# Optimization experiments

Measured on AMD Instinct MI355X. Metric: run time of the kernel, lower is better.

Reference implementation:

```python
import jax, jax.numpy as jnp
import numpy as np

KAPPA = 5.0
EPS_NORM = 1e-12  # torch F.normalize eps
EPS_LOG = 1e-09


def setup_inputs() -> dict:
    key = jax.random.key(0)
    student_output = jax.random.normal(key, (16384, 256), dtype=jnp.float32)
    return {"student_output": student_output}


def reference(student_output) -> jnp.ndarray:
    # L2-normalize rows (matches F.normalize: x / max(||x||, eps))
    norm = jnp.linalg.norm(student_output, axis=-1, keepdims=True)
    x_norm = student_output / jnp.maximum(norm, EPS_NORM)
    # pairwise cosine similarity [n, n]
    sim = x_norm @ x_norm.T
    kernel = jnp.exp(KAPPA * sim)
    density_estimates = kernel.sum(axis=1)  # [n]
    entropy = -jnp.mean(jnp.log(density_estimates + EPS_LOG))
    return entropy
```

## Files before the change

### kernel.cpp

```cpp
#include <hip/hip_runtime.h>


#define NROWS 16384
#define KDIM 256
#define NTILE 128
#define NT (NROWS / NTILE)
#define NSTRIP 8
#define TOTAL_BLOCKS (NT * NSTRIP)

#define SQRT_KLOG2E 2.68579577857f

typedef int i32x4_t __attribute__((ext_vector_type(4)));
typedef int i32x8_t __attribute__((ext_vector_type(8)));
typedef float f32x16_t __attribute__((ext_vector_type(16)));
typedef __attribute__((address_space(1))) const void global_cvoid_t;
typedef __attribute__((address_space(3))) void lds_void_t;

#if __has_builtin(__builtin_amdgcn_exp2f)
#define EXP2(x) __builtin_amdgcn_exp2f(x)
#else
#define EXP2(x) exp2f(x)
#endif

union frag8 { i32x8_t v8; i32x4_t v4[2]; };

__global__ __launch_bounds__(256)
void kde_normalize(const float* __restrict__ X, unsigned int* __restrict__ Xn8,
                   float* __restrict__ density, unsigned int* __restrict__ ticket) {
  const int wave = threadIdx.x >> 6;
  const int lane = threadIdx.x & 63;
  const int row = blockIdx.x * 4 + wave;
  const float4 v = ((const float4*)(X + (size_t)row * KDIM))[lane];
  float ss = v.x * v.x + v.y * v.y + v.z * v.z + v.w * v.w;
  ss += __shfl_xor(ss, 1);
  ss += __shfl_xor(ss, 2);
  ss += __shfl_xor(ss, 4);
  ss += __shfl_xor(ss, 8);
  ss += __shfl_xor(ss, 16);
  ss += __shfl_xor(ss, 32);
  const float scale = SQRT_KLOG2E / fmaxf(sqrtf(ss), 1e-12f);
  int p = 0;
  p = __builtin_amdgcn_cvt_pk_fp8_f32(v.x * scale, v.y * scale, p, false);
  p = __builtin_amdgcn_cvt_pk_fp8_f32(v.z * scale, v.w * scale, p, true);
  Xn8[(size_t)row * 64 + lane] = (unsigned int)p;
  if (threadIdx.x < 4) density[blockIdx.x * 4 + threadIdx.x] = 0.0f;
  if (blockIdx.x == 0 && threadIdx.x == 0) *ticket = 0u;
}

__global__ __launch_bounds__(512, 4)
void kde_gemm(const unsigned char* __restrict__ Xn8, float* __restrict__ density,
              unsigned int* __restrict__ ticket, float* __restrict__ out) {
  extern __shared__ char smem[];
  char* buf = smem;

  const int tid = threadIdx.x;
  const int wave = tid >> 6;
  const int lane = tid & 63;
  const int wr = wave >> 1;
  const int wc = wave & 1;
  const int m32 = lane & 31;
  const int h = lane >> 5;
  const int bi = blockIdx.x;
  const int s = blockIdx.y;
  const int t0 = s * 8;
  const int nt = (s == 0 && bi < NT / 2) ? 9 : 8;
  const char* Xb = (const char*)Xn8;

#define STAGE(base_row)                                                           \
  for (int c = wave; c < 32; c += 8) {                                            \
    const int rt = c >> 3, kb = (c >> 1) & 3, hh = c & 1;                         \
    const size_t gofs =                                                           \
        (size_t)((base_row) + rt * 32 + m32) * KDIM + kb * 64 + h * 32 + hh * 16; \
    __builtin_amdgcn_global_load_lds((global_cvoid_t*)(Xb + gofs),                \
                                     (lds_void_t*)(buf + c * 1024), 16, 0, 0);    \
  }

  STAGE(bi * NTILE);
  __syncthreads();
  frag8 areg[4];
#pragma unroll
  for (int kb = 0; kb < 4; kb++) {
    const char* pa = buf + (wr * 8 + kb * 2) * 1024 + lane * 16;
    areg[kb].v4[0] = *(const i32x4_t*)pa;
    areg[kb].v4[1] = *(const i32x4_t*)(pa + 1024);
  }
  __syncthreads();

  float rs[16];
#pragma unroll
  for (int r = 0; r < 16; r++) rs[r] = 0.0f;

  for (int k = 0; k < nt; ++k) {
    const int t = (k == 8) ? 64 : t0 + k;
    const int J = (bi + t) & (NT - 1);

    STAGE(J * NTILE);
    __syncthreads();

    f32x16_t acc[2];
#pragma unroll
    for (int j = 0; j < 2; j++) acc[j] = (f32x16_t)0.0f;

#pragma unroll
    for (int kb = 0; kb < 4; ++kb) {
      frag8 bf[2];
#pragma unroll
      for (int j = 0; j < 2; j++) {
        const char* pb = buf + ((wc * 2 + j) * 8 + kb * 2) * 1024 + lane * 16;
        bf[j].v4[0] = *(const i32x4_t*)pb;
        bf[j].v4[1] = *(const i32x4_t*)(pb + 1024);
      }
#pragma unroll
      for (int j = 0; j < 2; j++)
        acc[j] = __builtin_amdgcn_mfma_scale_f32_32x32x64_f8f6f4(
            areg[kb].v8, bf[j].v8, acc[j], 0, 0, 0, 127, 0, 127);
    }

    float c0 = 0.0f, c1 = 0.0f;
#pragma unroll
    for (int r = 0; r < 16; r++) {
      const float e0 = EXP2(acc[0][r]);
      const float e1 = EXP2(acc[1][r]);
      rs[r] += e0 + e1;
      c0 += e0;
      c1 += e1;
    }

    if (t != 0) {
      c0 += __shfl_xor(c0, 32);
      c1 += __shfl_xor(c1, 32);
      if (h == 0) {
        atomicAdd(&density[J * NTILE + wc * 64 + m32], c0);
        atomicAdd(&density[J * NTILE + wc * 64 + 32 + m32], c1);
      }
    }

    __syncthreads();
  }

#pragma unroll
  for (int r = 0; r < 16; r++) {
    float v = rs[r];
    v += __shfl_xor(v, 1);
    v += __shfl_xor(v, 2);
    v += __shfl_xor(v, 4);
    v += __shfl_xor(v, 8);
    v += __shfl_xor(v, 16);
    if (m32 == 0) {
      const int row = bi * NTILE + wr * 32 + (r & 3) + 8 * (r >> 2) + 4 * h;
      atomicAdd(&density[row], v);
    }
  }
#undef STAGE

  __syncthreads();
  if (tid == 0) {
    __threadfence();
    ((volatile unsigned int*)smem)[0] = atomicAdd(ticket, 1u);
  }
  __syncthreads();
  if (((volatile unsigned int*)smem)[0] == TOTAL_BLOCKS - 1) {
    __threadfence();
    float ssum = 0.0f;
    for (int i = tid; i < NROWS; i += 512) {
      const float d = __hip_atomic_load(&density[i], __ATOMIC_RELAXED,
                                        __HIP_MEMORY_SCOPE_AGENT);
      ssum += logf(d + 1e-9f);
    }
    ssum += __shfl_xor(ssum, 1);
    ssum += __shfl_xor(ssum, 2);
    ssum += __shfl_xor(ssum, 4);
    ssum += __shfl_xor(ssum, 8);
    ssum += __shfl_xor(ssum, 16);
    ssum += __shfl_xor(ssum, 32);
    float* red = ((float*)smem) + 16;
    if (lane == 0) red[wave] = ssum;
    __syncthreads();
    if (tid == 0) {
      float tot = 0.0f;
      for (int w = 0; w < 8; w++) tot += red[w];
      out[0] = -tot / (float)NROWS;
    }
  }
}

extern "C" void kernel_launch(void* const* d_in, const int* in_sizes, int n_in,
                              void* d_out, int out_size, void* d_ws, size_t ws_size,
                              hipStream_t stream) {
  const float* X = (const float*)d_in[0];
  float* out = (float*)d_out;
  char* ws = (char*)d_ws;
  unsigned int* Xn8 = (unsigned int*)ws;
  float* density = (float*)(ws + (size_t)NROWS * KDIM);
  unsigned int* ticket = (unsigned int*)(density + NROWS);

  hipFuncSetAttribute((const void*)kde_gemm,
                      hipFuncAttributeMaxDynamicSharedMemorySize, 32768);

  kde_normalize<<<NROWS / 4, 256, 0, stream>>>(X, Xn8, density, ticket);
  kde_gemm<<<dim3(NT, NSTRIP), 512, 32768, stream>>>((const unsigned char*)ws,
                                                     density, ticket, out);
}
```

Measured before the change: 142.5 us.

## Use 256-row A tiles per block with double-buffered B staging

Each block now holds a 256-row A tile, with two wave groups of 128 rows each, and streams 128-row B tiles through two LDS buffers. The next tile is prefetched while the current one is computed, so the per-iteration stage-then-sync stall goes away. This reuses every staged B tile across twice as many A rows and halves the grid to 64x8 blocks. The symmetric triangle schedule is recomputed with per-group activity and diagonal masks. In exchange, LDS use doubles to 64KB, which may lower occupancy, and the triangle bookkeeping grows more complex.

```diff
diff --git a/kernel.cpp b/kernel.cpp
--- a/kernel.cpp
+++ b/kernel.cpp
@@ -3,10 +3,9 @@
 
 #define NROWS 16384
 #define KDIM 256
-#define NTILE 128
-#define NT (NROWS / NTILE)
+#define NT 128
 #define NSTRIP 8
-#define TOTAL_BLOCKS (NT * NSTRIP)
+#define TOTAL_BLOCKS (64 * NSTRIP)
 
 #define SQRT_KLOG2E 2.68579577857f
 
@@ -51,39 +50,52 @@
 void kde_gemm(const unsigned char* __restrict__ Xn8, float* __restrict__ density,
               unsigned int* __restrict__ ticket, float* __restrict__ out) {
   extern __shared__ char smem[];
-  char* buf = smem;
+  char* buf0 = smem;
+  char* buf1 = smem + 32768;
 
   const int tid = threadIdx.x;
   const int wave = tid >> 6;
   const int lane = tid & 63;
-  const int wr = wave >> 1;
-  const int wc = wave & 1;
+  const int g = wave >> 2;
+  const int wr2 = wave & 3;
   const int m32 = lane & 31;
   const int h = lane >> 5;
   const int bi = blockIdx.x;
   const int s = blockIdx.y;
-  const int t0 = s * 8;
-  const int nt = (s == 0 && bi < NT / 2) ? 9 : 8;
+  const bool lo = (bi < 32);
+  int t0, nt;
+  if (lo) { nt = (s < 2) ? 9 : 8; t0 = (s < 2) ? 9 * s : 18 + (s - 2) * 8; }
+  else    { nt = (s == 0) ? 9 : 8; t0 = (s == 0) ? 0 : 9 + (s - 1) * 8; }
+  const int tmax_g0 = lo ? 64 : 63;
+  const int tmax_g1 = lo ? 65 : 64;
   const char* Xb = (const char*)Xn8;
 
-#define STAGE(base_row)                                                           \
+#define STAGE(base_row, dst)                                                      \
   for (int c = wave; c < 32; c += 8) {                                            \
     const int rt = c >> 3, kb = (c >> 1) & 3, hh = c & 1;                         \
     const size_t gofs =                                                           \
         (size_t)((base_row) + rt * 32 + m32) * KDIM + kb * 64 + h * 32 + hh * 16; \
     __builtin_amdgcn_global_load_lds((global_cvoid_t*)(Xb + gofs),                \
-                                     (lds_void_t*)(buf + c * 1024), 16, 0, 0);    \
-  }
-
-  STAGE(bi * NTILE);
-  __syncthreads();
+                                     (lds_void_t*)((dst) + c * 1024), 16, 0, 0);  \
+  }
+
+  STAGE(bi * 256, buf0);
+  STAGE(bi * 256 + 128, buf1);
+  __syncthreads();
+
   frag8 areg[4];
-#pragma unroll
-  for (int kb = 0; kb < 4; kb++) {
-    const char* pa = buf + (wr * 8 + kb * 2) * 1024 + lane * 16;
-    areg[kb].v4[0] = *(const i32x4_t*)pa;
-    areg[kb].v4[1] = *(const i32x4_t*)(pa + 1024);
-  }
+  {
+    const char* ab = g ? buf1 : buf0;
+#pragma unroll
+    for (int kb = 0; kb < 4; kb++) {
+      const char* pa = ab + (wr2 * 8 + kb * 2) * 1024 + lane * 16;
+      areg[kb].v4[0] = *(const i32x4_t*)pa;
+      areg[kb].v4[1] = *(const i32x4_t*)(pa + 1024);
+    }
+  }
+  __syncthreads();
+
+  STAGE(((bi * 2 + t0) & (NT - 1)) * 128, buf0);
   __syncthreads();
 
   float rs[16];
@@ -91,47 +103,53 @@
   for (int r = 0; r < 16; r++) rs[r] = 0.0f;
 
   for (int k = 0; k < nt; ++k) {
-    const int t = (k == 8) ? 64 : t0 + k;
-    const int J = (bi + t) & (NT - 1);
-
-    STAGE(J * NTILE);
-    __syncthreads();
-
-    f32x16_t acc[2];
-#pragma unroll
-    for (int j = 0; j < 2; j++) acc[j] = (f32x16_t)0.0f;
-
-#pragma unroll
-    for (int kb = 0; kb < 4; ++kb) {
-      frag8 bf[2];
-#pragma unroll
-      for (int j = 0; j < 2; j++) {
-        const char* pb = buf + ((wc * 2 + j) * 8 + kb * 2) * 1024 + lane * 16;
-        bf[j].v4[0] = *(const i32x4_t*)pb;
-        bf[j].v4[1] = *(const i32x4_t*)(pb + 1024);
-      }
-#pragma unroll
-      for (int j = 0; j < 2; j++)
-        acc[j] = __builtin_amdgcn_mfma_scale_f32_32x32x64_f8f6f4(
-            areg[kb].v8, bf[j].v8, acc[j], 0, 0, 0, 127, 0, 127);
-    }
-
-    float c0 = 0.0f, c1 = 0.0f;
-#pragma unroll
-    for (int r = 0; r < 16; r++) {
-      const float e0 = EXP2(acc[0][r]);
-      const float e1 = EXP2(acc[1][r]);
-      rs[r] += e0 + e1;
-      c0 += e0;
-      c1 += e1;
-    }
-
-    if (t != 0) {
-      c0 += __shfl_xor(c0, 32);
-      c1 += __shfl_xor(c1, 32);
-      if (h == 0) {
-        atomicAdd(&density[J * NTILE + wc * 64 + m32], c0);
-        atomicAdd(&density[J * NTILE + wc * 64 + 32 + m32], c1);
+    const int t = t0 + k;
+    const int J = (bi * 2 + t) & (NT - 1);
+    char* rbuf = (k & 1) ? buf1 : buf0;
+    char* sbuf = (k & 1) ? buf0 : buf1;
+
+    if (k + 1 < nt) STAGE(((bi * 2 + t + 1) & (NT - 1)) * 128, sbuf);
+
+    const bool act = g ? (t >= 1 && t <= tmax_g1) : (t <= tmax_g0);
+    const bool diag = g ? (t == 1) : (t == 0);
+
+    if (act) {
+#pragma unroll
+      for (int jp = 0; jp < 2; ++jp) {
+        f32x16_t acc[2];
+        acc[0] = (f32x16_t)0.0f;
+        acc[1] = (f32x16_t)0.0f;
+#pragma unroll
+        for (int kb = 0; kb < 4; ++kb) {
+          frag8 bf[2];
+#pragma unroll
+          for (int j = 0; j < 2; j++) {
+            const char* pb = rbuf + ((jp * 2 + j) * 8 + kb * 2) * 1024 + lane * 16;
+            bf[j].v4[0] = *(const i32x4_t*)pb;
+            bf[j].v4[1] = *(const i32x4_t*)(pb + 1024);
+          }
+#pragma unroll
+          for (int j = 0; j < 2; j++)
+            acc[j] = __builtin_amdgcn_mfma_scale_f32_32x32x64_f8f6f4(
+                areg[kb].v8, bf[j].v8, acc[j], 0, 0, 0, 127, 0, 127);
+        }
+        float c0 = 0.0f, c1 = 0.0f;
+#pragma unroll
+        for (int r = 0; r < 16; r++) {
+          const float e0 = EXP2(acc[0][r]);
+          const float e1 = EXP2(acc[1][r]);
+          rs[r] += e0 + e1;
+          c0 += e0;
+          c1 += e1;
+        }
+        if (!diag) {
+          c0 += __shfl_xor(c0, 32);
+          c1 += __shfl_xor(c1, 32);
+          if (h == 0) {
+            atomicAdd(&density[J * 128 + (jp * 2 + 0) * 32 + m32], c0);
+            atomicAdd(&density[J * 128 + (jp * 2 + 1) * 32 + m32], c1);
+          }
+        }
       }
     }
 
@@ -147,7 +165,7 @@
     v += __shfl_xor(v, 8);
     v += __shfl_xor(v, 16);
     if (m32 == 0) {
-      const int row = bi * NTILE + wr * 32 + (r & 3) + 8 * (r >> 2) + 4 * h;
+      const int row = bi * 256 + g * 128 + wr2 * 32 + (r & 3) + 8 * (r >> 2) + 4 * h;
       atomicAdd(&density[row], v);
     }
   }
@@ -195,9 +213,9 @@
   unsigned int* ticket = (unsigned int*)(density + NROWS);
 
   hipFuncSetAttribute((const void*)kde_gemm,
-                      hipFuncAttributeMaxDynamicSharedMemorySize, 32768);
+                      hipFuncAttributeMaxDynamicSharedMemorySize, 65536);
 
   kde_normalize<<<NROWS / 4, 256, 0, stream>>>(X, Xn8, density, ticket);
-  kde_gemm<<<dim3(NT, NSTRIP), 512, 32768, stream>>>((const unsigned char*)ws,
+  kde_gemm<<<dim3(64, NSTRIP), 512, 65536, stream>>>((const unsigned char*)ws,
                                                      density, ticket, out);
 }
```

Measured after the change: 142.8 us. No clear change (+0.2%).
